# Performance work log

Measured on AMD Instinct MI355X. Metric: run time of the kernel, lower is better.

## Reference

```python
import jax, jax.numpy as jnp
import numpy as np
import math

D_MODEL = 512
NUM_HEADS = 8
D_K = D_MODEL // NUM_HEADS
MAX_LEN = 500
BATCH = 32
SEQ = 480


def setup_inputs() -> dict:
    key = jax.random.key(0)
    ks = jax.random.split(key, 10)
    s = 0.02
    x = jax.random.normal(ks[0], (BATCH, SEQ, D_MODEL), dtype=jnp.float32)
    wq = jax.random.normal(ks[1], (D_MODEL, D_MODEL), dtype=jnp.float32) * s
    bq = jnp.zeros((D_MODEL,), jnp.float32)
    wk = jax.random.normal(ks[2], (D_MODEL, D_MODEL), dtype=jnp.float32) * s
    bk = jnp.zeros((D_MODEL,), jnp.float32)
    wv = jax.random.normal(ks[3], (D_MODEL, D_MODEL), dtype=jnp.float32) * s
    bv = jnp.zeros((D_MODEL,), jnp.float32)
    wo = jax.random.normal(ks[4], (D_MODEL, D_MODEL), dtype=jnp.float32) * s
    bo = jnp.zeros((D_MODEL,), jnp.float32)
    rel_bias = jax.random.normal(ks[5], (NUM_HEADS, MAX_LEN, MAX_LEN), dtype=jnp.float32) * 0.02
    return {"x": x, "wq": wq, "bq": bq, "wk": wk, "bk": bk, "wv": wv,
            "bv": bv, "wo": wo, "bo": bo, "rel_bias": rel_bias}


def reference(x, wq, bq, wk, bk, wv, bv, wo, bo, rel_bias):
    B, S, D = x.shape
    H, dk = NUM_HEADS, D_K
    scale = math.sqrt(dk)
    # QKV projections -> [B, H, S, dk]
    q = (x @ wq + bq).reshape(B, S, H, dk).transpose(0, 2, 1, 3)
    k = (x @ wk + bk).reshape(B, S, H, dk).transpose(0, 2, 1, 3)
    v = (x @ wv + bv).reshape(B, S, H, dk).transpose(0, 2, 1, 3)
    scores = jnp.einsum('bhqd,bhkd->bhqk', q, k) / scale
    scores = scores + rel_bias[None, :, :S, :S]
    causal = jnp.triu(jnp.ones((S, S), dtype=bool), k=1)  # True where j > i
    scores = jnp.where(causal[None, None], -jnp.inf, scores)
    attn = jax.nn.softmax(scores, axis=-1)
    ctx = jnp.einsum('bhqk,bhkd->bhqd', attn, v)
    ctx = ctx.transpose(0, 2, 1, 3).reshape(B, S, D)
    out = ctx @ wo + bo
    return out, attn.mean(axis=1)
```

## Files before the change

kernel.cpp:

```cpp
#include <hip/hip_runtime.h>
#include <hip/hip_bf16.h>


typedef unsigned short ushort_t;
typedef __attribute__((ext_vector_type(8))) short short8;
typedef __attribute__((ext_vector_type(4))) float floatx4;

#define NB 32
#define NS 480
#define ND 512
#define NH 8
#define NDK 64
#define MAXLEN 500
#define KSTRIDE 72
#define BSTRIDE 68
#define PSTR 36

__device__ __forceinline__ ushort_t f2bf(float f) {
  union { float f; unsigned u; } v; v.f = f;
  unsigned r = v.u + 0x7FFFu + ((v.u >> 16) & 1u);
  return (ushort_t)(r >> 16);
}

#define GLOAD_LDS16(g, l)                                                      \
  __builtin_amdgcn_global_load_lds(                                            \
      (const __attribute__((address_space(1))) void*)(g),                      \
      (__attribute__((address_space(3))) void*)(l), 16, 0, 0)

__global__ void cvt_x(const float* __restrict__ x, ushort_t* __restrict__ xb) {
  int idx = blockIdx.x * 256 + threadIdx.x;
  float4 v = ((const float4*)x)[idx];
  ushort4 o;
  o.x = f2bf(v.x); o.y = f2bf(v.y); o.z = f2bf(v.z); o.w = f2bf(v.w);
  ((ushort4*)xb)[idx] = o;
}

__global__ void cvt_w(const float* __restrict__ wq, const float* __restrict__ wk,
                      const float* __restrict__ wv, const float* __restrict__ wo,
                      ushort_t* __restrict__ wqT, ushort_t* __restrict__ wkT,
                      ushort_t* __restrict__ wvT, ushort_t* __restrict__ woT) {
  __shared__ float t[32][33];
  int z = blockIdx.z;
  const float* w = (z == 0) ? wq : (z == 1) ? wk : (z == 2) ? wv : wo;
  ushort_t* wT = (z == 0) ? wqT : (z == 1) ? wkT : (z == 2) ? wvT : woT;
  int k0 = blockIdx.x * 32, n0 = blockIdx.y * 32;
  int tx = threadIdx.x & 31, ty = threadIdx.x >> 5;
#pragma unroll
  for (int yy = 0; yy < 4; ++yy)
    t[ty + yy * 8][tx] = w[(k0 + ty + yy * 8) * ND + n0 + tx];
  __syncthreads();
#pragma unroll
  for (int yy = 0; yy < 4; ++yy)
    wT[(n0 + ty + yy * 8) * ND + k0 + tx] = f2bf(t[tx][ty + yy * 8]);
}

__global__ void cvt_rbt(const float* __restrict__ rel_bias, float* __restrict__ rbt) {
  int kt = blockIdx.x, ib = blockIdx.y, h = blockIdx.z;
  int lm = threadIdx.x & 15, ii = threadIdx.x >> 4;
  int i = ib * 16 + ii;
  float f0 = rel_bias[((size_t)h * MAXLEN + i) * MAXLEN + kt * 32 + lm];
  float f1 = rel_bias[((size_t)h * MAXLEN + i) * MAXLEN + kt * 32 + 16 + lm];
  float2 o = {f0, f1};
  *(float2*)&rbt[(((size_t)h * 15 + kt) * NS + i) * 32 + 2 * lm] = o;
}

__global__ __launch_bounds__(256)
void qk_gemm(const ushort_t* __restrict__ xb,
             const ushort_t* __restrict__ wqT, const ushort_t* __restrict__ wkT,
             const float* __restrict__ bq, const float* __restrict__ bk,
             ushort_t* __restrict__ qb, ushort_t* __restrict__ kb) {
  __shared__ __align__(16) ushort_t sA[128 * 64];
  __shared__ __align__(16) ushort_t sB[128 * 64];
  const int tid = threadIdx.x;
  const int wid = tid >> 6, lane = tid & 63;
  const int lm = lane & 15, quad = lane >> 4;
  const int wr = wid >> 1, wc = wid & 1;
  const int row0 = blockIdx.x * 128;
  const int col0 = blockIdx.y * 128;
  const int z = blockIdx.z;
  const ushort_t* Bt = (z == 0) ? wqT : wkT;
  const float* bias = (z == 0) ? bq : bk;

  floatx4 zero4 = {0.f, 0.f, 0.f, 0.f};
  floatx4 acc[4][4];
#pragma unroll
  for (int i = 0; i < 4; ++i)
#pragma unroll
    for (int j = 0; j < 4; ++j) acc[i][j] = zero4;

  for (int k0 = 0; k0 < ND; k0 += 64) {
#pragma unroll
    for (int c = 0; c < 4; ++c) {
      int li = c * 256 + tid;
      int row = li >> 3, kc = li & 7;
      int kcs = kc ^ (row & 7);
      GLOAD_LDS16(xb + (row0 + row) * ND + k0 + kcs * 8, sA + (c * 256 + wid * 64) * 8);
      GLOAD_LDS16(Bt + (col0 + row) * ND + k0 + kcs * 8, sB + (c * 256 + wid * 64) * 8);
    }
    __syncthreads();
#pragma unroll
    for (int h2 = 0; h2 < 2; ++h2) {
      short8 a[4], b[4];
#pragma unroll
      for (int i = 0; i < 4; ++i) {
        int row = wr * 64 + i * 16 + lm;
        a[i] = *(const short8*)&sA[row * 64 + (((h2 << 2) | quad) ^ (lm & 7)) * 8];
      }
#pragma unroll
      for (int j = 0; j < 4; ++j) {
        int row = wc * 64 + j * 16 + lm;
        b[j] = *(const short8*)&sB[row * 64 + (((h2 << 2) | quad) ^ (lm & 7)) * 8];
      }
#pragma unroll
      for (int i = 0; i < 4; ++i)
#pragma unroll
        for (int j = 0; j < 4; ++j)
          acc[i][j] = __builtin_amdgcn_mfma_f32_16x16x32_bf16(a[i], b[j], acc[i][j], 0, 0, 0);
    }
    __syncthreads();
  }

  float bsv[4];
#pragma unroll
  for (int j = 0; j < 4; ++j) bsv[j] = bias[col0 + wc * 64 + j * 16 + lm];

#pragma unroll
  for (int i = 0; i < 4; ++i)
#pragma unroll
    for (int j = 0; j < 4; ++j)
#pragma unroll
      for (int r = 0; r < 4; ++r) {
        int m = row0 + wr * 64 + i * 16 + quad * 4 + r;
        int n = col0 + wc * 64 + j * 16 + lm;
        float val = acc[i][j][r] + bsv[j];
        int bb = m / NS, s = m - bb * NS;
        int h = n >> 6, d = n & 63;
        ushort_t o = f2bf(val);
        if (z == 0) qb[((bb * NH + h) * NS + s) * NDK + d] = o;
        else        kb[((bb * NH + h) * NS + s) * NDK + d] = o;
      }
}

__global__ __launch_bounds__(256)
void v_gemm(const ushort_t* __restrict__ xb, const ushort_t* __restrict__ wvT,
            const float* __restrict__ bv, ushort_t* __restrict__ vtil) {
  __shared__ __align__(16) ushort_t sA[128 * 64];
  __shared__ __align__(16) ushort_t sB[128 * 64];
  const int tid = threadIdx.x;
  const int wid = tid >> 6, lane = tid & 63;
  const int lm = lane & 15, quad = lane >> 4;
  const int wr = wid >> 1, wc = wid & 1;
  const int row0 = blockIdx.x * 128;
  const int col0 = blockIdx.y * 128;
  const int b = blockIdx.z;
  const ushort_t* xbb = xb + (size_t)b * NS * ND;

  floatx4 zero4 = {0.f, 0.f, 0.f, 0.f};
  floatx4 acc[4][4];
#pragma unroll
  for (int i = 0; i < 4; ++i)
#pragma unroll
    for (int j = 0; j < 4; ++j) acc[i][j] = zero4;

  for (int k0 = 0; k0 < ND; k0 += 64) {
#pragma unroll
    for (int c = 0; c < 4; ++c) {
      int li = c * 256 + tid;
      int row = li >> 3, kc = li & 7;
      int kcs = kc ^ (row & 7);
      GLOAD_LDS16(wvT + (row0 + row) * ND + k0 + kcs * 8, sA + (c * 256 + wid * 64) * 8);
      int srow = min(col0 + row, NS - 1);
      GLOAD_LDS16(xbb + srow * ND + k0 + kcs * 8, sB + (c * 256 + wid * 64) * 8);
    }
    __syncthreads();
#pragma unroll
    for (int h2 = 0; h2 < 2; ++h2) {
      short8 a[4], b2[4];
#pragma unroll
      for (int i = 0; i < 4; ++i) {
        int row = wr * 64 + i * 16 + lm;
        a[i] = *(const short8*)&sA[row * 64 + (((h2 << 2) | quad) ^ (lm & 7)) * 8];
      }
#pragma unroll
      for (int j = 0; j < 4; ++j) {
        int row = wc * 64 + j * 16 + lm;
        b2[j] = *(const short8*)&sB[row * 64 + (((h2 << 2) | quad) ^ (lm & 7)) * 8];
      }
#pragma unroll
      for (int i = 0; i < 4; ++i)
#pragma unroll
        for (int j = 0; j < 4; ++j)
          acc[i][j] = __builtin_amdgcn_mfma_f32_16x16x32_bf16(a[i], b2[j], acc[i][j], 0, 0, 0);
    }
    __syncthreads();
  }

#pragma unroll
  for (int i = 0; i < 4; ++i)
#pragma unroll
    for (int r = 0; r < 4; ++r) {
      int m = row0 + wr * 64 + i * 16 + quad * 4 + r;
      float bias = bv[m];
#pragma unroll
      for (int j = 0; j < 4; ++j) {
        int n = col0 + wc * 64 + j * 16 + lm;
        if (n < NS) {
          size_t idx = (((size_t)b * NH + (m >> 6)) * 15 + (n >> 5)) * 2048 +
                       (m & 63) * 32 + (n & 31);
          vtil[idx] = f2bf(acc[i][j][r] + bias);
        }
      }
    }
}

__global__ __launch_bounds__(256)
void flash_attn(const ushort_t* __restrict__ qb, const ushort_t* __restrict__ kb,
                const ushort_t* __restrict__ vtil, const float* __restrict__ rbt,
                ushort_t* __restrict__ ctxb, float* __restrict__ cst) {
  const int bh = blockIdx.x;
  const int b = bh >> 3, h = bh & 7;
  const int tid = threadIdx.x;
  const int wid = tid >> 6, lane = tid & 63;
  const int lm = lane & 15, quad = lane >> 4;

  __shared__ __align__(16) ushort_t sP[4][32 * PSTR];

  const int t = 14 - (blockIdx.y * 4 + wid);
  if (t < 0) return;
  const int nkt = t + 1;

  const ushort_t* qh = qb + (size_t)bh * NS * NDK;
  const ushort_t* kh = kb + (size_t)bh * NS * NDK;
  const ushort_t* vb = vtil + (size_t)bh * 15 * 2048;
  const float* rb = rbt + (size_t)h * 15 * NS * 32;

  short8 aq[2][2];
#pragma unroll
  for (int g = 0; g < 2; ++g) {
    aq[g][0] = *(const short8*)&qh[(t * 32 + g * 16 + lm) * NDK + quad * 8];
    aq[g][1] = *(const short8*)&qh[(t * 32 + g * 16 + lm) * NDK + 32 + quad * 8];
  }

  float lsum[2][4];
  floatx4 O[2][4];
  floatx4 zero4 = {0.f, 0.f, 0.f, 0.f};
#pragma unroll
  for (int g = 0; g < 2; ++g) {
#pragma unroll
    for (int r = 0; r < 4; ++r) lsum[g][r] = 0.f;
#pragma unroll
    for (int jd = 0; jd < 4; ++jd) O[g][jd] = zero4;
  }

  for (int kt = 0; kt < nkt; ++kt) {
    const int kvA = kt * 32 + lm;
    const int kvB = kvA + 16;
    short8 bkA0 = *(const short8*)&kh[kvA * NDK + quad * 8];
    short8 bkA1 = *(const short8*)&kh[kvA * NDK + 32 + quad * 8];
    short8 bkB0 = *(const short8*)&kh[kvB * NDK + quad * 8];
    short8 bkB1 = *(const short8*)&kh[kvB * NDK + 32 + quad * 8];
    short8 bv2[4];
#pragma unroll
    for (int jd = 0; jd < 4; ++jd)
      bv2[jd] = *(const short8*)&vb[kt * 2048 + (jd * 16 + lm) * 32 + quad * 8];

    floatx4 sA[2], sB[2];
#pragma unroll
    for (int g = 0; g < 2; ++g) {
      floatx4 s = zero4;
      s = __builtin_amdgcn_mfma_f32_16x16x32_bf16(aq[g][0], bkA0, s, 0, 0, 0);
      s = __builtin_amdgcn_mfma_f32_16x16x32_bf16(aq[g][1], bkA1, s, 0, 0, 0);
      sA[g] = s;
      s = zero4;
      s = __builtin_amdgcn_mfma_f32_16x16x32_bf16(aq[g][0], bkB0, s, 0, 0, 0);
      s = __builtin_amdgcn_mfma_f32_16x16x32_bf16(aq[g][1], bkB1, s, 0, 0, 0);
      sB[g] = s;
    }

#pragma unroll
    for (int g = 0; g < 2; ++g)
#pragma unroll
      for (int r = 0; r < 4; ++r) {
        int i = t * 32 + g * 16 + quad * 4 + r;
        float2 bb = *(const float2*)&rb[((size_t)kt * NS + i) * 32 + 2 * lm];
        float v0 = sA[g][r] * 0.125f + bb.x;
        float v1 = sB[g][r] * 0.125f + bb.y;
        if (kvA > i) v0 = -1e30f;
        if (kvB > i) v1 = -1e30f;
        float p0 = __expf(v0);
        float p1 = __expf(v1);
        lsum[g][r] += p0 + p1;
        sP[wid][(g * 16 + quad * 4 + r) * PSTR + lm] = f2bf(p0);
        sP[wid][(g * 16 + quad * 4 + r) * PSTR + 16 + lm] = f2bf(p1);
      }

#pragma unroll
    for (int g = 0; g < 2; ++g) {
      short8 ap = *(const short8*)&sP[wid][(g * 16 + lm) * PSTR + quad * 8];
#pragma unroll
      for (int jd = 0; jd < 4; ++jd)
        O[g][jd] = __builtin_amdgcn_mfma_f32_16x16x32_bf16(ap, bv2[jd], O[g][jd], 0, 0, 0);
    }
  }

#pragma unroll
  for (int off = 1; off < 16; off <<= 1)
#pragma unroll
    for (int g = 0; g < 2; ++g)
#pragma unroll
      for (int r = 0; r < 4; ++r) lsum[g][r] += __shfl_xor(lsum[g][r], off, 64);

#pragma unroll
  for (int g = 0; g < 2; ++g) {
    float rinv[4];
#pragma unroll
    for (int r = 0; r < 4; ++r) rinv[r] = 1.f / lsum[g][r];
#pragma unroll
    for (int jd = 0; jd < 4; ++jd)
#pragma unroll
      for (int r = 0; r < 4; ++r) {
        int i = t * 32 + g * 16 + quad * 4 + r;
        ctxb[((size_t)b * NS + i) * ND + h * NDK + jd * 16 + lm] =
            f2bf(O[g][jd][r] * rinv[r]);
      }
    if (lm == 0) {
#pragma unroll
      for (int r = 0; r < 4; ++r) {
        int i = t * 32 + g * 16 + quad * 4 + r;
        cst[((size_t)b * NS + i) * NH + h] = __logf(lsum[g][r]);
      }
    }
  }
}

__global__ __launch_bounds__(256)
void attn_mean_k(const ushort_t* __restrict__ qb, const ushort_t* __restrict__ kb,
                 const float* __restrict__ rel_bias, const float* __restrict__ cst,
                 float* __restrict__ attn_mean) {
  const int b = blockIdx.x;
  const int tile = blockIdx.y;
  const int it = tile >> 3, jt = tile & 7;
  const int tid = threadIdx.x;

  if (jt > it) {
    int r = tid >> 2;
    int i = it * 64 + r;
    if (i < NS) {
      float4 z = {0.f, 0.f, 0.f, 0.f};
#pragma unroll
      for (int cc = 0; cc < 4; ++cc) {
        int j = jt * 64 + (tid & 3) * 16 + cc * 4;
        if (j < NS) *(float4*)&attn_mean[((size_t)b * NS + i) * NS + j] = z;
      }
    }
    return;
  }

  __shared__ __align__(16) ushort_t sK[2][64 * KSTRIDE];
  __shared__ __align__(16) float sB[2][64 * BSTRIDE];

  const int wid = tid >> 6, lane = tid & 63;
  const int lm = lane & 15, quad = lane >> 4;
  const int i0 = it * 64 + wid * 16;
  const bool active = (i0 < NS);
  const int j0t = jt * 64;

  float cstv[4][8];
#pragma unroll
  for (int r = 0; r < 4; ++r) {
    int i = min(i0 + quad * 4 + r, NS - 1);
    float4 c0 = *(const float4*)&cst[((size_t)b * NS + i) * NH];
    float4 c1 = *(const float4*)&cst[((size_t)b * NS + i) * NH + 4];
    cstv[r][0] = c0.x; cstv[r][1] = c0.y; cstv[r][2] = c0.z; cstv[r][3] = c0.w;
    cstv[r][4] = c1.x; cstv[r][5] = c1.y; cstv[r][6] = c1.z; cstv[r][7] = c1.w;
  }

  const int krow0 = tid >> 3, koff = (tid & 7) * 8;
  const int brow0 = tid >> 4, boff = (tid & 15) * 4;
  const int kr0 = min(j0t + krow0, NS - 1);
  const int kr1 = min(j0t + krow0 + 32, NS - 1);

  uint4 kreg[2];
  float4 breg[4];
  short8 qa0, qa1, qn0, qn1;

  {
    const ushort_t* kh = kb + (size_t)(b * NH) * NS * NDK;
    kreg[0] = *(const uint4*)&kh[kr0 * NDK + koff];
    kreg[1] = *(const uint4*)&kh[kr1 * NDK + koff];
#pragma unroll
    for (int c = 0; c < 4; ++c) {
      int ri = min(it * 64 + brow0 + c * 16, NS - 1);
      breg[c] = *(const float4*)&rel_bias[((size_t)0 * MAXLEN + ri) * MAXLEN + j0t + boff];
    }
    const ushort_t* qh = qb + (size_t)(b * NH) * NS * NDK;
    int qi = min(i0 + lm, NS - 1);
    qa0 = *(const short8*)&qh[qi * NDK + quad * 8];
    qa1 = *(const short8*)&qh[qi * NDK + 32 + quad * 8];
    *(uint4*)&sK[0][krow0 * KSTRIDE + koff] = kreg[0];
    *(uint4*)&sK[0][(krow0 + 32) * KSTRIDE + koff] = kreg[1];
#pragma unroll
    for (int c = 0; c < 4; ++c)
      *(float4*)&sB[0][(brow0 + c * 16) * BSTRIDE + boff] = breg[c];
  }
  __syncthreads();

  floatx4 zero4 = {0.f, 0.f, 0.f, 0.f};
  floatx4 acc[4];
#pragma unroll
  for (int jj = 0; jj < 4; ++jj) acc[jj] = zero4;

#pragma unroll
  for (int h = 0; h < NH; ++h) {
    const int buf = h & 1;
    if (h < NH - 1) {
      const ushort_t* kh = kb + (size_t)(b * NH + h + 1) * NS * NDK;
      kreg[0] = *(const uint4*)&kh[kr0 * NDK + koff];
      kreg[1] = *(const uint4*)&kh[kr1 * NDK + koff];
#pragma unroll
      for (int c = 0; c < 4; ++c) {
        int ri = min(it * 64 + brow0 + c * 16, NS - 1);
        breg[c] = *(const float4*)&rel_bias[((size_t)(h + 1) * MAXLEN + ri) * MAXLEN +
                                            j0t + boff];
      }
      const ushort_t* qh = qb + (size_t)(b * NH + h + 1) * NS * NDK;
      int qi = min(i0 + lm, NS - 1);
      qn0 = *(const short8*)&qh[qi * NDK + quad * 8];
      qn1 = *(const short8*)&qh[qi * NDK + 32 + quad * 8];
    }

#pragma unroll
    for (int jj = 0; jj < 4; ++jj) {
      short8 bk0 = *(const short8*)&sK[buf][(jj * 16 + lm) * KSTRIDE + quad * 8];
      short8 bk1 = *(const short8*)&sK[buf][(jj * 16 + lm) * KSTRIDE + 32 + quad * 8];
      floatx4 s = zero4;
      s = __builtin_amdgcn_mfma_f32_16x16x32_bf16(qa0, bk0, s, 0, 0, 0);
      s = __builtin_amdgcn_mfma_f32_16x16x32_bf16(qa1, bk1, s, 0, 0, 0);
#pragma unroll
      for (int r = 0; r < 4; ++r) {
        float bias = sB[buf][(quad * 4 + r) * BSTRIDE + jj * 16 + lm];
        float p = __expf(s[r] * 0.125f + bias - cstv[r][h]);
        int i = i0 + quad * 4 + r;
        int j = j0t + jj * 16 + lm;
        if (j > i) p = 0.f;
        acc[jj][r] += p;
      }
    }

    if (h < NH - 1) {
      *(uint4*)&sK[buf ^ 1][krow0 * KSTRIDE + koff] = kreg[0];
      *(uint4*)&sK[buf ^ 1][(krow0 + 32) * KSTRIDE + koff] = kreg[1];
#pragma unroll
      for (int c = 0; c < 4; ++c)
        *(float4*)&sB[buf ^ 1][(brow0 + c * 16) * BSTRIDE + boff] = breg[c];
      qa0 = qn0; qa1 = qn1;
    }
    __syncthreads();
  }

  if (active) {
#pragma unroll
    for (int jj = 0; jj < 4; ++jj) {
      int j = j0t + jj * 16 + lm;
      if (j < NS) {
#pragma unroll
        for (int r = 0; r < 4; ++r)
          attn_mean[((size_t)b * NS + i0 + quad * 4 + r) * NS + j] =
              acc[jj][r] * 0.125f;
      }
    }
  }
}

__global__ __launch_bounds__(256)
void out_gemm(const ushort_t* __restrict__ ctxb, const ushort_t* __restrict__ woT,
              const float* __restrict__ bo, float* __restrict__ out) {
  __shared__ __align__(16) ushort_t sA[128 * 64];
  __shared__ __align__(16) ushort_t sB[128 * 64];
  const int tid = threadIdx.x;
  const int wid = tid >> 6, lane = tid & 63;
  const int lm = lane & 15, quad = lane >> 4;
  const int wr = wid >> 1, wc = wid & 1;
  const int row0 = blockIdx.x * 128;
  const int col0 = blockIdx.y * 128;

  floatx4 zero4 = {0.f, 0.f, 0.f, 0.f};
  floatx4 acc[4][4];
#pragma unroll
  for (int i = 0; i < 4; ++i)
#pragma unroll
    for (int j = 0; j < 4; ++j) acc[i][j] = zero4;

  for (int k0 = 0; k0 < ND; k0 += 64) {
#pragma unroll
    for (int c = 0; c < 4; ++c) {
      int li = c * 256 + tid;
      int row = li >> 3, kc = li & 7;
      int kcs = kc ^ (row & 7);
      GLOAD_LDS16(ctxb + (row0 + row) * ND + k0 + kcs * 8, sA + (c * 256 + wid * 64) * 8);
      GLOAD_LDS16(woT + (col0 + row) * ND + k0 + kcs * 8, sB + (c * 256 + wid * 64) * 8);
    }
    __syncthreads();
#pragma unroll
    for (int h2 = 0; h2 < 2; ++h2) {
      short8 a[4], b[4];
#pragma unroll
      for (int i = 0; i < 4; ++i) {
        int row = wr * 64 + i * 16 + lm;
        a[i] = *(const short8*)&sA[row * 64 + (((h2 << 2) | quad) ^ (lm & 7)) * 8];
      }
#pragma unroll
      for (int j = 0; j < 4; ++j) {
        int row = wc * 64 + j * 16 + lm;
        b[j] = *(const short8*)&sB[row * 64 + (((h2 << 2) | quad) ^ (lm & 7)) * 8];
      }
#pragma unroll
      for (int i = 0; i < 4; ++i)
#pragma unroll
        for (int j = 0; j < 4; ++j)
          acc[i][j] = __builtin_amdgcn_mfma_f32_16x16x32_bf16(a[i], b[j], acc[i][j], 0, 0, 0);
    }
    __syncthreads();
  }

  float bsv[4];
#pragma unroll
  for (int j = 0; j < 4; ++j) bsv[j] = bo[col0 + wc * 64 + j * 16 + lm];

#pragma unroll
  for (int i = 0; i < 4; ++i)
#pragma unroll
    for (int j = 0; j < 4; ++j)
#pragma unroll
      for (int r = 0; r < 4; ++r) {
        int m = row0 + wr * 64 + i * 16 + quad * 4 + r;
        int n = col0 + wc * 64 + j * 16 + lm;
        out[m * ND + n] = acc[i][j][r] + bsv[j];
      }
}

extern "C" void kernel_launch(void* const* d_in, const int* in_sizes, int n_in,
                              void* d_out, int out_size, void* d_ws, size_t ws_size,
                              hipStream_t stream) {
  const float* x  = (const float*)d_in[0];
  const float* wq = (const float*)d_in[1];
  const float* bq = (const float*)d_in[2];
  const float* wk = (const float*)d_in[3];
  const float* bk = (const float*)d_in[4];
  const float* wv = (const float*)d_in[5];
  const float* bv = (const float*)d_in[6];
  const float* wo = (const float*)d_in[7];
  const float* bo = (const float*)d_in[8];
  const float* rel_bias = (const float*)d_in[9];

  char* w = (char*)d_ws;
  ushort_t* xb  = (ushort_t*)w;
  ushort_t* wqT = (ushort_t*)(w + 15728640);
  ushort_t* wkT = wqT + 262144;
  ushort_t* wvT = wkT + 262144;
  ushort_t* woT = wvT + 262144;
  ushort_t* qb  = (ushort_t*)(w + 15728640 + 4 * 524288);
  ushort_t* kb  = qb + 7864320;
  ushort_t* vtil = kb + 7864320;
  ushort_t* ctxb = vtil + 7864320;
  float* cstat = (float*)(w + 15728640 + 4 * 524288 + 4 * 15728640);
  float* rbt = (float*)w;

  float* out0 = (float*)d_out;
  float* attn_mean = out0 + 7864320;

  cvt_x<<<dim3(7680), dim3(256), 0, stream>>>(x, xb);
  cvt_w<<<dim3(16, 16, 4), dim3(256), 0, stream>>>(wq, wk, wv, wo, wqT, wkT, wvT, woT);
  qk_gemm<<<dim3(120, 4, 2), dim3(256), 0, stream>>>(xb, wqT, wkT, bq, bk, qb, kb);
  v_gemm<<<dim3(4, 4, 32), dim3(256), 0, stream>>>(xb, wvT, bv, vtil);
  cvt_rbt<<<dim3(15, 30, 8), dim3(256), 0, stream>>>(rel_bias, rbt);
  flash_attn<<<dim3(256, 4), dim3(256), 0, stream>>>(qb, kb, vtil, rbt, ctxb, cstat);
  attn_mean_k<<<dim3(32, 64), dim3(256), 0, stream>>>(qb, kb, rel_bias, cstat,
                                                      attn_mean);
  out_gemm<<<dim3(120, 4), dim3(256), 0, stream>>>(ctxb, woT, bo, out0);
}
```

Before: 252.5 us.

## Store fp16 probabilities in flash_attn and reduce head-mean from scratch instead of recomputing

flash_attn now writes its unnormalized exp probabilities as packed fp16 to a scratch buffer, plus the per-row inverse sum. A new lightweight kernel averages those over heads to form attn_mean, replacing the kernel that recomputed QK^T, bias and exp for every head. The change also switches to exp2 with the log2e factor folded into the scale and bias, applies the causal mask only on diagonal tiles, and software-pipelines the K/V loads with double buffering under launch_bounds(256,3). The cost is a large extra scratch write and read, and fp16 storage of probabilities loses some precision.

```diff
diff --git a/kernel.cpp b/kernel.cpp
--- a/kernel.cpp
+++ b/kernel.cpp
@@ -5,6 +5,7 @@
 typedef unsigned short ushort_t;
 typedef __attribute__((ext_vector_type(8))) short short8;
 typedef __attribute__((ext_vector_type(4))) float floatx4;
+typedef __attribute__((ext_vector_type(2))) __fp16 half2v;
 
 #define NB 32
 #define NS 480
@@ -12,9 +13,8 @@
 #define NH 8
 #define NDK 64
 #define MAXLEN 500
-#define KSTRIDE 72
-#define BSTRIDE 68
 #define PSTR 36
+#define SCL 0.18033688f
 
 __device__ __forceinline__ ushort_t f2bf(float f) {
   union { float f; unsigned u; } v; v.f = f;
@@ -58,8 +58,8 @@
   int kt = blockIdx.x, ib = blockIdx.y, h = blockIdx.z;
   int lm = threadIdx.x & 15, ii = threadIdx.x >> 4;
   int i = ib * 16 + ii;
-  float f0 = rel_bias[((size_t)h * MAXLEN + i) * MAXLEN + kt * 32 + lm];
-  float f1 = rel_bias[((size_t)h * MAXLEN + i) * MAXLEN + kt * 32 + 16 + lm];
+  float f0 = rel_bias[((size_t)h * MAXLEN + i) * MAXLEN + kt * 32 + lm] * 1.44269504f;
+  float f1 = rel_bias[((size_t)h * MAXLEN + i) * MAXLEN + kt * 32 + 16 + lm] * 1.44269504f;
   float2 o = {f0, f1};
   *(float2*)&rbt[(((size_t)h * 15 + kt) * NS + i) * 32 + 2 * lm] = o;
 }
@@ -213,10 +213,11 @@
     }
 }
 
-__global__ __launch_bounds__(256)
+__global__ __launch_bounds__(256, 3)
 void flash_attn(const ushort_t* __restrict__ qb, const ushort_t* __restrict__ kb,
                 const ushort_t* __restrict__ vtil, const float* __restrict__ rbt,
-                ushort_t* __restrict__ ctxb, float* __restrict__ cst) {
+                ushort_t* __restrict__ ctxb, float* __restrict__ cst,
+                unsigned* __restrict__ pscr) {
   const int bh = blockIdx.x;
   const int b = bh >> 3, h = bh & 7;
   const int tid = threadIdx.x;
@@ -233,6 +234,7 @@
   const ushort_t* kh = kb + (size_t)bh * NS * NDK;
   const ushort_t* vb = vtil + (size_t)bh * 15 * 2048;
   const float* rb = rbt + (size_t)h * 15 * NS * 32;
+  unsigned* pp = pscr + ((size_t)(bh * 120 + (t * (t + 1)) / 2) * 64 + lane) * 8;
 
   short8 aq[2][2];
 #pragma unroll
@@ -252,55 +254,88 @@
     for (int jd = 0; jd < 4; ++jd) O[g][jd] = zero4;
   }
 
-  for (int kt = 0; kt < nkt; ++kt) {
-    const int kvA = kt * 32 + lm;
-    const int kvB = kvA + 16;
-    short8 bkA0 = *(const short8*)&kh[kvA * NDK + quad * 8];
-    short8 bkA1 = *(const short8*)&kh[kvA * NDK + 32 + quad * 8];
-    short8 bkB0 = *(const short8*)&kh[kvB * NDK + quad * 8];
-    short8 bkB1 = *(const short8*)&kh[kvB * NDK + 32 + quad * 8];
-    short8 bv2[4];
+  auto loadKV = [&](int kt_, short8& kA0_, short8& kA1_, short8& kB0_,
+                    short8& kB1_, short8* vv_) {
+    int ra = (kt_ * 32 + lm) * NDK;
+    int rbx = ra + 16 * NDK;
+    kA0_ = *(const short8*)&kh[ra + quad * 8];
+    kA1_ = *(const short8*)&kh[ra + 32 + quad * 8];
+    kB0_ = *(const short8*)&kh[rbx + quad * 8];
+    kB1_ = *(const short8*)&kh[rbx + 32 + quad * 8];
 #pragma unroll
     for (int jd = 0; jd < 4; ++jd)
-      bv2[jd] = *(const short8*)&vb[kt * 2048 + (jd * 16 + lm) * 32 + quad * 8];
+      vv_[jd] = *(const short8*)&vb[kt_ * 2048 + (jd * 16 + lm) * 32 + quad * 8];
+  };
+
+  auto compute = [&](int kt_, short8 kA0_, short8 kA1_, short8 kB0_,
+                     short8 kB1_, const short8* vv_) {
+    float2 bb[2][4];
+#pragma unroll
+    for (int g = 0; g < 2; ++g)
+#pragma unroll
+      for (int r = 0; r < 4; ++r) {
+        int i = t * 32 + g * 16 + quad * 4 + r;
+        bb[g][r] = *(const float2*)&rb[((size_t)kt_ * NS + i) * 32 + 2 * lm];
+      }
 
     floatx4 sA[2], sB[2];
 #pragma unroll
     for (int g = 0; g < 2; ++g) {
       floatx4 s = zero4;
-      s = __builtin_amdgcn_mfma_f32_16x16x32_bf16(aq[g][0], bkA0, s, 0, 0, 0);
-      s = __builtin_amdgcn_mfma_f32_16x16x32_bf16(aq[g][1], bkA1, s, 0, 0, 0);
+      s = __builtin_amdgcn_mfma_f32_16x16x32_bf16(aq[g][0], kA0_, s, 0, 0, 0);
+      s = __builtin_amdgcn_mfma_f32_16x16x32_bf16(aq[g][1], kA1_, s, 0, 0, 0);
       sA[g] = s;
       s = zero4;
-      s = __builtin_amdgcn_mfma_f32_16x16x32_bf16(aq[g][0], bkB0, s, 0, 0, 0);
-      s = __builtin_amdgcn_mfma_f32_16x16x32_bf16(aq[g][1], bkB1, s, 0, 0, 0);
+      s = __builtin_amdgcn_mfma_f32_16x16x32_bf16(aq[g][0], kB0_, s, 0, 0, 0);
+      s = __builtin_amdgcn_mfma_f32_16x16x32_bf16(aq[g][1], kB1_, s, 0, 0, 0);
       sB[g] = s;
     }
 
-#pragma unroll
-    for (int g = 0; g < 2; ++g)
-#pragma unroll
-      for (int r = 0; r < 4; ++r) {
-        int i = t * 32 + g * 16 + quad * 4 + r;
-        float2 bb = *(const float2*)&rb[((size_t)kt * NS + i) * 32 + 2 * lm];
-        float v0 = sA[g][r] * 0.125f + bb.x;
-        float v1 = sB[g][r] * 0.125f + bb.y;
-        if (kvA > i) v0 = -1e30f;
-        if (kvB > i) v1 = -1e30f;
-        float p0 = __expf(v0);
-        float p1 = __expf(v1);
+    const bool diag = (kt_ == t);
+#pragma unroll
+    for (int g = 0; g < 2; ++g) {
+      unsigned pw[4];
+#pragma unroll
+      for (int r = 0; r < 4; ++r) {
+        float p0 = __builtin_amdgcn_exp2f(fmaf(sA[g][r], SCL, bb[g][r].x));
+        float p1 = __builtin_amdgcn_exp2f(fmaf(sB[g][r], SCL, bb[g][r].y));
+        if (diag) {
+          int i = t * 32 + g * 16 + quad * 4 + r;
+          if (kt_ * 32 + lm > i) p0 = 0.f;
+          if (kt_ * 32 + 16 + lm > i) p1 = 0.f;
+        }
         lsum[g][r] += p0 + p1;
-        sP[wid][(g * 16 + quad * 4 + r) * PSTR + lm] = f2bf(p0);
-        sP[wid][(g * 16 + quad * 4 + r) * PSTR + 16 + lm] = f2bf(p1);
-      }
+        unsigned pk;
+        asm("v_cvt_pk_bf16_f32 %0, %1, %2" : "=v"(pk) : "v"(p0), "v"(p1));
+        sP[wid][(g * 16 + quad * 4 + r) * PSTR + lm] = (ushort_t)(pk & 0xffffu);
+        sP[wid][(g * 16 + quad * 4 + r) * PSTR + 16 + lm] = (ushort_t)(pk >> 16);
+        half2v hp = __builtin_amdgcn_cvt_pkrtz(p0, p1);
+        pw[r] = *(unsigned*)&hp;
+      }
+      uint4 pq = {pw[0], pw[1], pw[2], pw[3]};
+      *(uint4*)(pp + (size_t)kt_ * 512 + g * 4) = pq;
+    }
 
 #pragma unroll
     for (int g = 0; g < 2; ++g) {
       short8 ap = *(const short8*)&sP[wid][(g * 16 + lm) * PSTR + quad * 8];
 #pragma unroll
       for (int jd = 0; jd < 4; ++jd)
-        O[g][jd] = __builtin_amdgcn_mfma_f32_16x16x32_bf16(ap, bv2[jd], O[g][jd], 0, 0, 0);
-    }
+        O[g][jd] = __builtin_amdgcn_mfma_f32_16x16x32_bf16(ap, vv_[jd], O[g][jd], 0, 0, 0);
+    }
+  };
+
+  short8 kA0a, kA1a, kB0a, kB1a, va[4];
+  short8 kA0b, kA1b, kB0b, kB1b, vbf[4];
+  loadKV(0, kA0a, kA1a, kB0a, kB1a, va);
+  int kt = 0;
+  while (true) {
+    if (kt + 1 < nkt) loadKV(kt + 1, kA0b, kA1b, kB0b, kB1b, vbf);
+    compute(kt, kA0a, kA1a, kB0a, kB1a, va);
+    if (++kt >= nkt) break;
+    if (kt + 1 < nkt) loadKV(kt + 1, kA0a, kA1a, kB0a, kB1a, va);
+    compute(kt, kA0b, kA1b, kB0b, kB1b, vbf);
+    if (++kt >= nkt) break;
   }
 
 #pragma unroll
@@ -327,149 +362,65 @@
 #pragma unroll
       for (int r = 0; r < 4; ++r) {
         int i = t * 32 + g * 16 + quad * 4 + r;
-        cst[((size_t)b * NS + i) * NH + h] = __logf(lsum[g][r]);
-      }
-    }
-  }
-}
-
-__global__ __launch_bounds__(256)
-void attn_mean_k(const ushort_t* __restrict__ qb, const ushort_t* __restrict__ kb,
-                 const float* __restrict__ rel_bias, const float* __restrict__ cst,
-                 float* __restrict__ attn_mean) {
-  const int b = blockIdx.x;
-  const int tile = blockIdx.y;
-  const int it = tile >> 3, jt = tile & 7;
-  const int tid = threadIdx.x;
-
-  if (jt > it) {
-    int r = tid >> 2;
-    int i = it * 64 + r;
-    if (i < NS) {
-      float4 z = {0.f, 0.f, 0.f, 0.f};
-#pragma unroll
-      for (int cc = 0; cc < 4; ++cc) {
-        int j = jt * 64 + (tid & 3) * 16 + cc * 4;
-        if (j < NS) *(float4*)&attn_mean[((size_t)b * NS + i) * NS + j] = z;
-      }
-    }
+        cst[(size_t)bh * NS + i] = rinv[r];
+      }
+    }
+  }
+}
+
+__global__ __launch_bounds__(64)
+void attn_mean_p(const unsigned* __restrict__ pscr, const float* __restrict__ cst,
+                 float* __restrict__ am) {
+  const int b = blockIdx.x, t = blockIdx.y, kt = blockIdx.z;
+  const int lane = threadIdx.x;
+  const int lm = lane & 15, quad = lane >> 4;
+  float* outp = am + ((size_t)b * NS + t * 32) * NS + (size_t)kt * 32;
+  if (kt > t) {
+#pragma unroll
+    for (int g = 0; g < 2; ++g)
+#pragma unroll
+      for (int r = 0; r < 4; ++r) {
+        int row = g * 16 + quad * 4 + r;
+        outp[(size_t)row * NS + lm] = 0.f;
+        outp[(size_t)row * NS + 16 + lm] = 0.f;
+      }
     return;
   }
-
-  __shared__ __align__(16) ushort_t sK[2][64 * KSTRIDE];
-  __shared__ __align__(16) float sB[2][64 * BSTRIDE];
-
-  const int wid = tid >> 6, lane = tid & 63;
-  const int lm = lane & 15, quad = lane >> 4;
-  const int i0 = it * 64 + wid * 16;
-  const bool active = (i0 < NS);
-  const int j0t = jt * 64;
-
-  float cstv[4][8];
-#pragma unroll
-  for (int r = 0; r < 4; ++r) {
-    int i = min(i0 + quad * 4 + r, NS - 1);
-    float4 c0 = *(const float4*)&cst[((size_t)b * NS + i) * NH];
-    float4 c1 = *(const float4*)&cst[((size_t)b * NS + i) * NH + 4];
-    cstv[r][0] = c0.x; cstv[r][1] = c0.y; cstv[r][2] = c0.z; cstv[r][3] = c0.w;
-    cstv[r][4] = c1.x; cstv[r][5] = c1.y; cstv[r][6] = c1.z; cstv[r][7] = c1.w;
-  }
-
-  const int krow0 = tid >> 3, koff = (tid & 7) * 8;
-  const int brow0 = tid >> 4, boff = (tid & 15) * 4;
-  const int kr0 = min(j0t + krow0, NS - 1);
-  const int kr1 = min(j0t + krow0 + 32, NS - 1);
-
-  uint4 kreg[2];
-  float4 breg[4];
-  short8 qa0, qa1, qn0, qn1;
-
-  {
-    const ushort_t* kh = kb + (size_t)(b * NH) * NS * NDK;
-    kreg[0] = *(const uint4*)&kh[kr0 * NDK + koff];
-    kreg[1] = *(const uint4*)&kh[kr1 * NDK + koff];
-#pragma unroll
-    for (int c = 0; c < 4; ++c) {
-      int ri = min(it * 64 + brow0 + c * 16, NS - 1);
-      breg[c] = *(const float4*)&rel_bias[((size_t)0 * MAXLEN + ri) * MAXLEN + j0t + boff];
-    }
-    const ushort_t* qh = qb + (size_t)(b * NH) * NS * NDK;
-    int qi = min(i0 + lm, NS - 1);
-    qa0 = *(const short8*)&qh[qi * NDK + quad * 8];
-    qa1 = *(const short8*)&qh[qi * NDK + 32 + quad * 8];
-    *(uint4*)&sK[0][krow0 * KSTRIDE + koff] = kreg[0];
-    *(uint4*)&sK[0][(krow0 + 32) * KSTRIDE + koff] = kreg[1];
-#pragma unroll
-    for (int c = 0; c < 4; ++c)
-      *(float4*)&sB[0][(brow0 + c * 16) * BSTRIDE + boff] = breg[c];
-  }
-  __syncthreads();
-
-  floatx4 zero4 = {0.f, 0.f, 0.f, 0.f};
-  floatx4 acc[4];
-#pragma unroll
-  for (int jj = 0; jj < 4; ++jj) acc[jj] = zero4;
+  const int m = (t * (t + 1)) / 2 + kt;
+  float a0[2][4], a1[2][4];
+#pragma unroll
+  for (int g = 0; g < 2; ++g)
+#pragma unroll
+    for (int r = 0; r < 4; ++r) { a0[g][r] = 0.f; a1[g][r] = 0.f; }
 
 #pragma unroll
   for (int h = 0; h < NH; ++h) {
-    const int buf = h & 1;
-    if (h < NH - 1) {
-      const ushort_t* kh = kb + (size_t)(b * NH + h + 1) * NS * NDK;
-      kreg[0] = *(const uint4*)&kh[kr0 * NDK + koff];
-      kreg[1] = *(const uint4*)&kh[kr1 * NDK + koff];
-#pragma unroll
-      for (int c = 0; c < 4; ++c) {
-        int ri = min(it * 64 + brow0 + c * 16, NS - 1);
-        breg[c] = *(const float4*)&rel_bias[((size_t)(h + 1) * MAXLEN + ri) * MAXLEN +
-                                            j0t + boff];
-      }
-      const ushort_t* qh = qb + (size_t)(b * NH + h + 1) * NS * NDK;
-      int qi = min(i0 + lm, NS - 1);
-      qn0 = *(const short8*)&qh[qi * NDK + quad * 8];
-      qn1 = *(const short8*)&qh[qi * NDK + 32 + quad * 8];
-    }
-
-#pragma unroll
-    for (int jj = 0; jj < 4; ++jj) {
-      short8 bk0 = *(const short8*)&sK[buf][(jj * 16 + lm) * KSTRIDE + quad * 8];
-      short8 bk1 = *(const short8*)&sK[buf][(jj * 16 + lm) * KSTRIDE + 32 + quad * 8];
-      floatx4 s = zero4;
-      s = __builtin_amdgcn_mfma_f32_16x16x32_bf16(qa0, bk0, s, 0, 0, 0);
-      s = __builtin_amdgcn_mfma_f32_16x16x32_bf16(qa1, bk1, s, 0, 0, 0);
-#pragma unroll
-      for (int r = 0; r < 4; ++r) {
-        float bias = sB[buf][(quad * 4 + r) * BSTRIDE + jj * 16 + lm];
-        float p = __expf(s[r] * 0.125f + bias - cstv[r][h]);
-        int i = i0 + quad * 4 + r;
-        int j = j0t + jj * 16 + lm;
-        if (j > i) p = 0.f;
-        acc[jj][r] += p;
-      }
-    }
-
-    if (h < NH - 1) {
-      *(uint4*)&sK[buf ^ 1][krow0 * KSTRIDE + koff] = kreg[0];
-      *(uint4*)&sK[buf ^ 1][(krow0 + 32) * KSTRIDE + koff] = kreg[1];
-#pragma unroll
-      for (int c = 0; c < 4; ++c)
-        *(float4*)&sB[buf ^ 1][(brow0 + c * 16) * BSTRIDE + boff] = breg[c];
-      qa0 = qn0; qa1 = qn1;
-    }
-    __syncthreads();
-  }
-
-  if (active) {
-#pragma unroll
-    for (int jj = 0; jj < 4; ++jj) {
-      int j = j0t + jj * 16 + lm;
-      if (j < NS) {
-#pragma unroll
-        for (int r = 0; r < 4; ++r)
-          attn_mean[((size_t)b * NS + i0 + quad * 4 + r) * NS + j] =
-              acc[jj][r] * 0.125f;
-      }
-    }
-  }
+    const unsigned* pp = pscr + (((size_t)(b * NH + h) * 120 + m) * 64 + lane) * 8;
+    unsigned pu[8];
+    *(uint4*)&pu[0] = *(const uint4*)pp;
+    *(uint4*)&pu[4] = *(const uint4*)(pp + 4);
+    const float* cp = cst + (size_t)(b * NH + h) * NS + t * 32 + quad * 4;
+    float4 rv0 = *(const float4*)cp;
+    float4 rv1 = *(const float4*)(cp + 16);
+    float rv[8] = {rv0.x, rv0.y, rv0.z, rv0.w, rv1.x, rv1.y, rv1.z, rv1.w};
+#pragma unroll
+    for (int g = 0; g < 2; ++g)
+#pragma unroll
+      for (int r = 0; r < 4; ++r) {
+        half2v hp = *(half2v*)&pu[g * 4 + r];
+        a0[g][r] = fmaf((float)hp.x, rv[g * 4 + r], a0[g][r]);
+        a1[g][r] = fmaf((float)hp.y, rv[g * 4 + r], a1[g][r]);
+      }
+  }
+
+#pragma unroll
+  for (int g = 0; g < 2; ++g)
+#pragma unroll
+    for (int r = 0; r < 4; ++r) {
+      int row = g * 16 + quad * 4 + r;
+      outp[(size_t)row * NS + lm] = a0[g][r] * 0.125f;
+      outp[(size_t)row * NS + 16 + lm] = a1[g][r] * 0.125f;
+    }
 }
 
 __global__ __launch_bounds__(256)
@@ -563,7 +514,8 @@
   ushort_t* kb  = qb + 7864320;
   ushort_t* vtil = kb + 7864320;
   ushort_t* ctxb = vtil + 7864320;
-  float* cstat = (float*)(w + 15728640 + 4 * 524288 + 4 * 15728640);
+  float* cstat = (float*)(w + 80740352);
+  unsigned* pscr = (unsigned*)(w + 81264640);
   float* rbt = (float*)w;
 
   float* out0 = (float*)d_out;
@@ -574,8 +526,7 @@
   qk_gemm<<<dim3(120, 4, 2), dim3(256), 0, stream>>>(xb, wqT, wkT, bq, bk, qb, kb);
   v_gemm<<<dim3(4, 4, 32), dim3(256), 0, stream>>>(xb, wvT, bv, vtil);
   cvt_rbt<<<dim3(15, 30, 8), dim3(256), 0, stream>>>(rel_bias, rbt);
-  flash_attn<<<dim3(256, 4), dim3(256), 0, stream>>>(qb, kb, vtil, rbt, ctxb, cstat);
-  attn_mean_k<<<dim3(32, 64), dim3(256), 0, stream>>>(qb, kb, rel_bias, cstat,
-                                                      attn_mean);
+  flash_attn<<<dim3(256, 4), dim3(256), 0, stream>>>(qb, kb, vtil, rbt, ctxb, cstat, pscr);
+  attn_mean_p<<<dim3(32, 15, 15), dim3(64), 0, stream>>>(pscr, cstat, attn_mean);
   out_gemm<<<dim3(120, 4), dim3(256), 0, stream>>>(ctxb, woT, bo, out0);
 }
```

Result: slower. 269.0 us (+6.5%).

## Switch softmax to exp2 domain, reuse pre-tiled bias in attn_mean, split causal path

Applied to the files above, without the earlier changes.

The relative bias is pre-scaled by log2(e) when it is retiled, so both attention kernels can compute probabilities with a single fma plus a hardware exp2, and the log-sum statistic is stored in base 2. The flash kernel hoists its bias loads ahead of the MFMAs, skips causal masking on fully unmasked key tiles, packs the two bf16 conversions into one instruction, and raises wave priority around the MFMA blocks. attn_mean_k2 reads the bias directly from the retiled rbt buffer in registers instead of staging rel_bias through LDS, which removes that shared-memory traffic. The trade-offs are more live registers and several scattered global loads per head inside the loop.

```diff
diff --git a/kernel.cpp b/kernel.cpp
--- a/kernel.cpp
+++ b/kernel.cpp
@@ -13,8 +13,8 @@
 #define NDK 64
 #define MAXLEN 500
 #define KSTRIDE 72
-#define BSTRIDE 68
 #define PSTR 36
+#define SCL 0.18033688f
 
 __device__ __forceinline__ ushort_t f2bf(float f) {
   union { float f; unsigned u; } v; v.f = f;
@@ -58,8 +58,8 @@
   int kt = blockIdx.x, ib = blockIdx.y, h = blockIdx.z;
   int lm = threadIdx.x & 15, ii = threadIdx.x >> 4;
   int i = ib * 16 + ii;
-  float f0 = rel_bias[((size_t)h * MAXLEN + i) * MAXLEN + kt * 32 + lm];
-  float f1 = rel_bias[((size_t)h * MAXLEN + i) * MAXLEN + kt * 32 + 16 + lm];
+  float f0 = rel_bias[((size_t)h * MAXLEN + i) * MAXLEN + kt * 32 + lm] * 1.44269504f;
+  float f1 = rel_bias[((size_t)h * MAXLEN + i) * MAXLEN + kt * 32 + 16 + lm] * 1.44269504f;
   float2 o = {f0, f1};
   *(float2*)&rbt[(((size_t)h * 15 + kt) * NS + i) * 32 + 2 * lm] = o;
 }
@@ -263,8 +263,17 @@
 #pragma unroll
     for (int jd = 0; jd < 4; ++jd)
       bv2[jd] = *(const short8*)&vb[kt * 2048 + (jd * 16 + lm) * 32 + quad * 8];
+    float2 bb[2][4];
+#pragma unroll
+    for (int g = 0; g < 2; ++g)
+#pragma unroll
+      for (int r = 0; r < 4; ++r) {
+        int i = t * 32 + g * 16 + quad * 4 + r;
+        bb[g][r] = *(const float2*)&rb[((size_t)kt * NS + i) * 32 + 2 * lm];
+      }
 
     floatx4 sA[2], sB[2];
+    __builtin_amdgcn_s_setprio(1);
 #pragma unroll
     for (int g = 0; g < 2; ++g) {
       floatx4 s = zero4;
@@ -276,24 +285,40 @@
       s = __builtin_amdgcn_mfma_f32_16x16x32_bf16(aq[g][1], bkB1, s, 0, 0, 0);
       sB[g] = s;
     }
-
-#pragma unroll
-    for (int g = 0; g < 2; ++g)
-#pragma unroll
-      for (int r = 0; r < 4; ++r) {
-        int i = t * 32 + g * 16 + quad * 4 + r;
-        float2 bb = *(const float2*)&rb[((size_t)kt * NS + i) * 32 + 2 * lm];
-        float v0 = sA[g][r] * 0.125f + bb.x;
-        float v1 = sB[g][r] * 0.125f + bb.y;
-        if (kvA > i) v0 = -1e30f;
-        if (kvB > i) v1 = -1e30f;
-        float p0 = __expf(v0);
-        float p1 = __expf(v1);
-        lsum[g][r] += p0 + p1;
-        sP[wid][(g * 16 + quad * 4 + r) * PSTR + lm] = f2bf(p0);
-        sP[wid][(g * 16 + quad * 4 + r) * PSTR + 16 + lm] = f2bf(p1);
-      }
-
+    __builtin_amdgcn_s_setprio(0);
+
+    if (kt < t) {
+#pragma unroll
+      for (int g = 0; g < 2; ++g)
+#pragma unroll
+        for (int r = 0; r < 4; ++r) {
+          float p0 = __builtin_amdgcn_exp2f(fmaf(sA[g][r], SCL, bb[g][r].x));
+          float p1 = __builtin_amdgcn_exp2f(fmaf(sB[g][r], SCL, bb[g][r].y));
+          lsum[g][r] += p0 + p1;
+          unsigned pk;
+          asm("v_cvt_pk_bf16_f32 %0, %1, %2" : "=v"(pk) : "v"(p0), "v"(p1));
+          sP[wid][(g * 16 + quad * 4 + r) * PSTR + lm] = (ushort_t)(pk & 0xffffu);
+          sP[wid][(g * 16 + quad * 4 + r) * PSTR + 16 + lm] = (ushort_t)(pk >> 16);
+        }
+    } else {
+#pragma unroll
+      for (int g = 0; g < 2; ++g)
+#pragma unroll
+        for (int r = 0; r < 4; ++r) {
+          int i = t * 32 + g * 16 + quad * 4 + r;
+          float p0 = __builtin_amdgcn_exp2f(fmaf(sA[g][r], SCL, bb[g][r].x));
+          float p1 = __builtin_amdgcn_exp2f(fmaf(sB[g][r], SCL, bb[g][r].y));
+          if (kvA > i) p0 = 0.f;
+          if (kvB > i) p1 = 0.f;
+          lsum[g][r] += p0 + p1;
+          unsigned pk;
+          asm("v_cvt_pk_bf16_f32 %0, %1, %2" : "=v"(pk) : "v"(p0), "v"(p1));
+          sP[wid][(g * 16 + quad * 4 + r) * PSTR + lm] = (ushort_t)(pk & 0xffffu);
+          sP[wid][(g * 16 + quad * 4 + r) * PSTR + 16 + lm] = (ushort_t)(pk >> 16);
+        }
+    }
+
+    __builtin_amdgcn_s_setprio(1);
 #pragma unroll
     for (int g = 0; g < 2; ++g) {
       short8 ap = *(const short8*)&sP[wid][(g * 16 + lm) * PSTR + quad * 8];
@@ -301,6 +326,7 @@
       for (int jd = 0; jd < 4; ++jd)
         O[g][jd] = __builtin_amdgcn_mfma_f32_16x16x32_bf16(ap, bv2[jd], O[g][jd], 0, 0, 0);
     }
+    __builtin_amdgcn_s_setprio(0);
   }
 
 #pragma unroll
@@ -327,16 +353,16 @@
 #pragma unroll
       for (int r = 0; r < 4; ++r) {
         int i = t * 32 + g * 16 + quad * 4 + r;
-        cst[((size_t)b * NS + i) * NH + h] = __logf(lsum[g][r]);
+        cst[((size_t)b * NS + i) * NH + h] = __log2f(lsum[g][r]);
       }
     }
   }
 }
 
 __global__ __launch_bounds__(256)
-void attn_mean_k(const ushort_t* __restrict__ qb, const ushort_t* __restrict__ kb,
-                 const float* __restrict__ rel_bias, const float* __restrict__ cst,
-                 float* __restrict__ attn_mean) {
+void attn_mean_k2(const ushort_t* __restrict__ qb, const ushort_t* __restrict__ kb,
+                  const float* __restrict__ rbt, const float* __restrict__ cst,
+                  float* __restrict__ am) {
   const int b = blockIdx.x;
   const int tile = blockIdx.y;
   const int it = tile >> 3, jt = tile & 7;
@@ -350,58 +376,46 @@
 #pragma unroll
       for (int cc = 0; cc < 4; ++cc) {
         int j = jt * 64 + (tid & 3) * 16 + cc * 4;
-        if (j < NS) *(float4*)&attn_mean[((size_t)b * NS + i) * NS + j] = z;
+        if (j < NS) *(float4*)&am[((size_t)b * NS + i) * NS + j] = z;
       }
     }
     return;
   }
 
   __shared__ __align__(16) ushort_t sK[2][64 * KSTRIDE];
-  __shared__ __align__(16) float sB[2][64 * BSTRIDE];
 
   const int wid = tid >> 6, lane = tid & 63;
   const int lm = lane & 15, quad = lane >> 4;
   const int i0 = it * 64 + wid * 16;
   const bool active = (i0 < NS);
   const int j0t = jt * 64;
-
-  float cstv[4][8];
+  const int iq = min(i0 + lm, NS - 1);
+
+  int irow[4], ic[4];
 #pragma unroll
   for (int r = 0; r < 4; ++r) {
-    int i = min(i0 + quad * 4 + r, NS - 1);
-    float4 c0 = *(const float4*)&cst[((size_t)b * NS + i) * NH];
-    float4 c1 = *(const float4*)&cst[((size_t)b * NS + i) * NH + 4];
-    cstv[r][0] = c0.x; cstv[r][1] = c0.y; cstv[r][2] = c0.z; cstv[r][3] = c0.w;
-    cstv[r][4] = c1.x; cstv[r][5] = c1.y; cstv[r][6] = c1.z; cstv[r][7] = c1.w;
-  }
+    irow[r] = i0 + quad * 4 + r;
+    ic[r] = min(irow[r], NS - 1);
+  }
+  const int kt2g0 = j0t >> 5;
+  const int kt2g1 = min(kt2g0 + 1, 14);
 
   const int krow0 = tid >> 3, koff = (tid & 7) * 8;
-  const int brow0 = tid >> 4, boff = (tid & 15) * 4;
   const int kr0 = min(j0t + krow0, NS - 1);
   const int kr1 = min(j0t + krow0 + 32, NS - 1);
 
   uint4 kreg[2];
-  float4 breg[4];
   short8 qa0, qa1, qn0, qn1;
 
   {
     const ushort_t* kh = kb + (size_t)(b * NH) * NS * NDK;
     kreg[0] = *(const uint4*)&kh[kr0 * NDK + koff];
     kreg[1] = *(const uint4*)&kh[kr1 * NDK + koff];
-#pragma unroll
-    for (int c = 0; c < 4; ++c) {
-      int ri = min(it * 64 + brow0 + c * 16, NS - 1);
-      breg[c] = *(const float4*)&rel_bias[((size_t)0 * MAXLEN + ri) * MAXLEN + j0t + boff];
-    }
     const ushort_t* qh = qb + (size_t)(b * NH) * NS * NDK;
-    int qi = min(i0 + lm, NS - 1);
-    qa0 = *(const short8*)&qh[qi * NDK + quad * 8];
-    qa1 = *(const short8*)&qh[qi * NDK + 32 + quad * 8];
+    qa0 = *(const short8*)&qh[iq * NDK + quad * 8];
+    qa1 = *(const short8*)&qh[iq * NDK + 32 + quad * 8];
     *(uint4*)&sK[0][krow0 * KSTRIDE + koff] = kreg[0];
     *(uint4*)&sK[0][(krow0 + 32) * KSTRIDE + koff] = kreg[1];
-#pragma unroll
-    for (int c = 0; c < 4; ++c)
-      *(float4*)&sB[0][(brow0 + c * 16) * BSTRIDE + boff] = breg[c];
   }
   __syncthreads();
 
@@ -417,16 +431,18 @@
       const ushort_t* kh = kb + (size_t)(b * NH + h + 1) * NS * NDK;
       kreg[0] = *(const uint4*)&kh[kr0 * NDK + koff];
       kreg[1] = *(const uint4*)&kh[kr1 * NDK + koff];
-#pragma unroll
-      for (int c = 0; c < 4; ++c) {
-        int ri = min(it * 64 + brow0 + c * 16, NS - 1);
-        breg[c] = *(const float4*)&rel_bias[((size_t)(h + 1) * MAXLEN + ri) * MAXLEN +
-                                            j0t + boff];
-      }
       const ushort_t* qh = qb + (size_t)(b * NH + h + 1) * NS * NDK;
-      int qi = min(i0 + lm, NS - 1);
-      qn0 = *(const short8*)&qh[qi * NDK + quad * 8];
-      qn1 = *(const short8*)&qh[qi * NDK + 32 + quad * 8];
+      qn0 = *(const short8*)&qh[iq * NDK + quad * 8];
+      qn1 = *(const short8*)&qh[iq * NDK + 32 + quad * 8];
+    }
+
+    float2 b0[4], b1[4];
+    float c2[4];
+#pragma unroll
+    for (int r = 0; r < 4; ++r) {
+      c2[r] = cst[((size_t)b * NS + ic[r]) * NH + h];
+      b0[r] = *(const float2*)&rbt[(((size_t)h * 15 + kt2g0) * NS + ic[r]) * 32 + 2 * lm];
+      b1[r] = *(const float2*)&rbt[(((size_t)h * 15 + kt2g1) * NS + ic[r]) * 32 + 2 * lm];
     }
 
 #pragma unroll
@@ -434,15 +450,17 @@
       short8 bk0 = *(const short8*)&sK[buf][(jj * 16 + lm) * KSTRIDE + quad * 8];
       short8 bk1 = *(const short8*)&sK[buf][(jj * 16 + lm) * KSTRIDE + 32 + quad * 8];
       floatx4 s = zero4;
+      __builtin_amdgcn_s_setprio(1);
       s = __builtin_amdgcn_mfma_f32_16x16x32_bf16(qa0, bk0, s, 0, 0, 0);
       s = __builtin_amdgcn_mfma_f32_16x16x32_bf16(qa1, bk1, s, 0, 0, 0);
+      __builtin_amdgcn_s_setprio(0);
+      int j = j0t + jj * 16 + lm;
 #pragma unroll
       for (int r = 0; r < 4; ++r) {
-        float bias = sB[buf][(quad * 4 + r) * BSTRIDE + jj * 16 + lm];
-        float p = __expf(s[r] * 0.125f + bias - cstv[r][h]);
-        int i = i0 + quad * 4 + r;
-        int j = j0t + jj * 16 + lm;
-        if (j > i) p = 0.f;
+        float bsel = (jj == 0) ? b0[r].x : (jj == 1) ? b0[r].y
+                   : (jj == 2) ? b1[r].x : b1[r].y;
+        float p = __builtin_amdgcn_exp2f(fmaf(s[r], SCL, bsel - c2[r]));
+        if (j > irow[r]) p = 0.f;
         acc[jj][r] += p;
       }
     }
@@ -450,9 +468,6 @@
     if (h < NH - 1) {
       *(uint4*)&sK[buf ^ 1][krow0 * KSTRIDE + koff] = kreg[0];
       *(uint4*)&sK[buf ^ 1][(krow0 + 32) * KSTRIDE + koff] = kreg[1];
-#pragma unroll
-      for (int c = 0; c < 4; ++c)
-        *(float4*)&sB[buf ^ 1][(brow0 + c * 16) * BSTRIDE + boff] = breg[c];
       qa0 = qn0; qa1 = qn1;
     }
     __syncthreads();
@@ -465,8 +480,7 @@
       if (j < NS) {
 #pragma unroll
         for (int r = 0; r < 4; ++r)
-          attn_mean[((size_t)b * NS + i0 + quad * 4 + r) * NS + j] =
-              acc[jj][r] * 0.125f;
+          am[((size_t)b * NS + irow[r]) * NS + j] = acc[jj][r] * 0.125f;
       }
     }
   }
@@ -563,7 +577,7 @@
   ushort_t* kb  = qb + 7864320;
   ushort_t* vtil = kb + 7864320;
   ushort_t* ctxb = vtil + 7864320;
-  float* cstat = (float*)(w + 15728640 + 4 * 524288 + 4 * 15728640);
+  float* cstat = (float*)(w + 80740352);
   float* rbt = (float*)w;
 
   float* out0 = (float*)d_out;
@@ -575,7 +589,6 @@
   v_gemm<<<dim3(4, 4, 32), dim3(256), 0, stream>>>(xb, wvT, bv, vtil);
   cvt_rbt<<<dim3(15, 30, 8), dim3(256), 0, stream>>>(rel_bias, rbt);
   flash_attn<<<dim3(256, 4), dim3(256), 0, stream>>>(qb, kb, vtil, rbt, ctxb, cstat);
-  attn_mean_k<<<dim3(32, 64), dim3(256), 0, stream>>>(qb, kb, rel_bias, cstat,
-                                                      attn_mean);
+  attn_mean_k2<<<dim3(32, 64), dim3(256), 0, stream>>>(qb, kb, rbt, cstat, attn_mean);
   out_gemm<<<dim3(120, 4), dim3(256), 0, stream>>>(ctxb, woT, bo, out0);
 }
```

Result: no change. 252.2 us (-0.1%).
